# Optimization experiments

Hardware: AMD Instinct MI355X
Metric: run time of the kernel (lower is better)

Reference implementation:

```python
import jax, jax.numpy as jnp
import numpy as np

N_CIRC, N_MI, N_DIS = 40000, 15000, 8000
F_IN, HID, HEADS, OUT = 128, 64, 4, 64
E_CM, E_MD, E_CD = 400000, 300000, 300000
SIZES = (N_CIRC, N_MI, N_DIS)
# relation r: (src_type, dst_type) indices into [circ, mi, dis]
RELS = [(0, 1), (1, 2), (0, 2), (1, 0), (2, 1), (2, 0)]
EDGE_N = [E_CM, E_MD, E_CD, E_CM, E_MD, E_CD]


def _edges(k, n_src, n_dst, n_e):
    k1, k2 = jax.random.split(k)
    src = jax.random.randint(k1, (n_e,), 0, n_src, dtype=jnp.int32)
    dst = jax.random.randint(k2, (n_e,), 0, n_dst, dtype=jnp.int32)
    return jnp.stack([src, dst])


def setup_inputs() -> dict:
    key = jax.random.key(0)
    ks = jax.random.split(key, 20)
    x_circ = jax.random.normal(ks[0], (N_CIRC, F_IN), jnp.float32)
    x_mi = jax.random.normal(ks[1], (N_MI, F_IN), jnp.float32)
    x_dis = jax.random.normal(ks[2], (N_DIS, F_IN), jnp.float32)
    ed = [_edges(ks[3 + r], SIZES[RELS[r][0]], SIZES[RELS[r][1]], EDGE_N[r]) for r in range(6)]
    s1 = 1.0 / np.sqrt(F_IN)
    s2 = 1.0 / np.sqrt(HID * HEADS)
    W1 = jax.random.normal(ks[10], (6, F_IN, HEADS * HID), jnp.float32) * s1
    as1 = jax.random.normal(ks[11], (6, HEADS, HID), jnp.float32) * s2
    ad1 = jax.random.normal(ks[12], (6, HEADS, HID), jnp.float32) * s2
    b1 = jnp.zeros((6, HEADS * HID), jnp.float32)
    W2 = jax.random.normal(ks[13], (6, HEADS * HID, OUT), jnp.float32) * s2
    as2 = jax.random.normal(ks[14], (6, 1, OUT), jnp.float32) * s2
    ad2 = jax.random.normal(ks[15], (6, 1, OUT), jnp.float32) * s2
    b2 = jnp.zeros((6, OUT), jnp.float32)
    return {"x_circ": x_circ, "x_mi": x_mi, "x_dis": x_dis,
            "e_cm": ed[0], "e_md": ed[1], "e_cd": ed[2],
            "e_mc": ed[3], "e_dm": ed[4], "e_dc": ed[5],
            "W1": W1, "as1": as1, "ad1": ad1, "b1": b1,
            "W2": W2, "as2": as2, "ad2": ad2, "b2": b2}


def _gat(x_src, x_dst, src, dst, W, a_s, a_d, b, n_dst, concat):
    # PyG GATConv (shared lin for src/dst), add_self_loops=False, eval mode.
    H, C = a_s.shape
    h_src = (x_src @ W).reshape(-1, H, C)   # [Ns,H,C]
    h_dst = (x_dst @ W).reshape(-1, H, C)   # [Nd,H,C]
    al_s = jnp.einsum('nhc,hc->nh', h_src, a_s)
    al_d = jnp.einsum('nhc,hc->nh', h_dst, a_d)
    e = jax.nn.leaky_relu(al_s[src] + al_d[dst], 0.2)           # [E,H]
    m = jax.ops.segment_max(e, dst, num_segments=n_dst)         # [Nd,H]
    m = jnp.where(jnp.isfinite(m), m, 0.0)
    ex = jnp.exp(e - m[dst])
    den = jax.ops.segment_sum(ex, dst, num_segments=n_dst)
    alpha = ex / (den[dst] + 1e-16)                             # scatter-softmax
    msg = h_src[src] * alpha[:, :, None]                        # [E,H,C]
    out = jax.ops.segment_sum(msg.reshape(-1, H * C), dst, num_segments=n_dst)
    out = out.reshape(n_dst, H, C)
    return (out.reshape(n_dst, H * C) if concat else out.mean(axis=1)) + b


def _hetero(xs, edges, W, a_s, a_d, b, concat):
    acc = [[] for _ in xs]
    for r, (s, d) in enumerate(RELS):
        o = _gat(xs[s], xs[d], edges[r][0], edges[r][1], W[r], a_s[r], a_d[r], b[r], SIZES[d], concat)
        acc[d].append(o)
    return [jnp.mean(jnp.stack(lst), axis=0) for lst in acc]  # aggr='mean'


def reference(x_circ, x_mi, x_dis, e_cm, e_md, e_cd, e_mc, e_dm, e_dc,
              W1, as1, ad1, b1, W2, as2, ad2, b2):
    xs = [x_circ, x_mi, x_dis]
    edges = [e_cm, e_md, e_cd, e_mc, e_dm, e_dc]
    h = _hetero(xs, edges, W1, as1, ad1, b1, concat=True)
    h = [jax.nn.elu(v) for v in h]  # dropout is identity in eval
    h = _hetero(h, edges, W2, as2, ad2, b2, concat=False)
    out = [v / jnp.maximum(jnp.linalg.norm(v, axis=1, keepdims=True), 1e-12) for v in h]
    return tuple(out)
```

## Files before the change

kernel.cpp:

```cpp
#include <hip/hip_runtime.h>
#include <hip/hip_bf16.h>
#include <math.h>

#define NCIRC 40000
#define NMI   15000
#define NDIS  8000
#define NTOT  (NCIRC + NMI + NDIS)
#define OFFSTR 40064

typedef __hip_bfloat16 bf16;
typedef __attribute__((ext_vector_type(8))) short short8;
typedef __attribute__((ext_vector_type(4))) float f32x4;
typedef __attribute__((ext_vector_type(8))) unsigned short us8v;

static __device__ __forceinline__ float us2f(unsigned short u){ return __uint_as_float(((unsigned)u) << 16); }
static __device__ __forceinline__ unsigned short f2bu(float v){
    bf16 t = __float2bfloat16(v);
    return *reinterpret_cast<unsigned short*>(&t);
}
static __device__ __forceinline__ float ldx(const void* p, size_t i, int f32){
    return f32 ? ((const float*)p)[i] : __bfloat162float(((const bf16*)p)[i]);
}
static inline unsigned cdiv(long long a, long long b){ return (unsigned)((a + b - 1) / b); }

struct CsrArgs {
    const int* src[6]; const int* dst[6];
    int ecnt[6]; int eoff[6]; int nd[6];
};
struct Al1Args { const void* x[3]; const float* wa[3][4]; float* out[3][4]; int nt[3]; };
struct Al2Args { const unsigned short* x[3]; const float* wa[3][4]; float* out[3][4]; int nt[3]; };
struct GemmArgs { const void* A[6]; unsigned long long bOff[6]; unsigned long long cOff[6];
                  int M[6]; int nblk[6]; };
struct GatArgs {
    const unsigned short* srcs[3][2]; const int* off[3][2];
    const float* als[3][2]; const float* ald[3][2];
    const unsigned short* hs[3][2];
};
struct P1Args {
    CsrArgs ca;
    const void *W1, *as1, *ad1, *W2, *as2, *ad2, *b1, *b2;
    float *WA1S, *WA1D, *WA2S, *WA2D, *BIAS1, *BIAS2;
    bf16 *W1T, *W2T;
    int *CNT;
    int eTw1, eTw2, eWa1, eWa2, eBias;
    int nbCnt[6];
};
struct P2Args {
    CsrArgs ca;
    const int* OFF; int* POS; unsigned short* SRCS;
    GemmArgs g1;
    Al1Args a1;
    int eFill, eGemm;
    int nbCnt[6];
    int nbAl[3];
};
struct P3Args {
    Al2Args a2;
    GemmArgs g2;
    int eAl2;
    int nbAl[3];
};
struct P2ArgsFix { P2Args p; const bf16* W1T; bf16* HS1; };
struct P3ArgsFix { P3Args p; const bf16* W2T; bf16* HS2; };

__global__ void detect_dtype(const unsigned short* __restrict__ u, int* __restrict__ flag){
    int bad = 0;
    for (int i = threadIdx.x; i < 4096; i += 256){
        int e = (u[i] >> 7) & 0xFF;
        if (e >= 0x90) bad = 1;
    }
    if (bad) atomicOr(flag, 1);
}

static __device__ __forceinline__ void tw_body(const void* W, int f32, bf16* WT,
                                               int Kd, int Nd, int nrel, int blk){
    long long idx = (long long)blk * 256 + threadIdx.x;
    long long tot = (long long)nrel * Kd * Nd;
    if (idx >= tot) return;
    int per = Kd * Nd;
    int r = (int)(idx / per);
    int rem = (int)(idx % per);
    int n = rem / Kd, k = rem % Kd;
    float v = ldx(W, (size_t)r*per + (size_t)k*Nd + n, f32);
    WT[idx] = __float2bfloat16(v);
}

static __device__ __forceinline__ void wa1_body(const void* W1, const void* as1, const void* ad1,
                                                int f32, float* wa_s, float* wa_d, int blk){
    int r = blk >> 1;
    int t = (blk & 1)*256 + threadIdx.x;
    int f = t >> 2, h = t & 3;
    size_t wb = (size_t)r*128*256 + (size_t)f*256 + h*64;
    size_t ab = (size_t)r*256 + h*64;
    float ss = 0.f, sd = 0.f;
    for (int c = 0; c < 64; c++){
        float w = ldx(W1, wb + c, f32);
        ss += w * ldx(as1, ab + c, f32);
        sd += w * ldx(ad1, ab + c, f32);
    }
    wa_s[r*512 + t] = ss; wa_d[r*512 + t] = sd;
}

static __device__ __forceinline__ void wa2_body(const void* W2, const void* as2, const void* ad2,
                                                int f32, float* wa_s, float* wa_d, int r){
    int f = threadIdx.x;
    size_t wb = (size_t)r*256*64 + (size_t)f*64;
    float ss = 0.f, sd = 0.f;
    for (int c = 0; c < 64; c++){
        float w = ldx(W2, wb + c, f32);
        ss += w * ldx(as2, (size_t)r*64 + c, f32);
        sd += w * ldx(ad2, (size_t)r*64 + c, f32);
    }
    wa_s[r*256 + f] = ss; wa_d[r*256 + f] = sd;
}

static __device__ __forceinline__ void bias_body(const void* b1, const void* b2, int f32,
                                                 float* BIAS1, float* BIAS2, int t){
    const int relA[3] = {3, 0, 1};
    const int relB[3] = {5, 4, 2};
    int c = threadIdx.x;
    BIAS1[t*256 + c] = 0.5f*(ldx(b1, relA[t]*256 + c, f32) + ldx(b1, relB[t]*256 + c, f32));
    if (c < 64)
        BIAS2[t*64 + c] = 0.5f*(ldx(b2, relA[t]*64 + c, f32) + ldx(b2, relB[t]*64 + c, f32));
}

static __device__ void al1_body(const Al1Args& a, int f32, int t, int blk, float (*swa)[512]){
    int N = a.nt[t];
    for (int i = threadIdx.x; i < 2048; i += 256) swa[i >> 9][i & 511] = a.wa[t][i >> 9][i & 511];
    __syncthreads();
    int n = blk * 256 + threadIdx.x;
    if (n >= N) return;
    float s[4][4] = {};
    if (f32){
        const float* xr = (const float*)a.x[t] + (size_t)n*128;
        for (int f = 0; f < 128; f++){
            float v = xr[f];
            #pragma unroll
            for (int j = 0; j < 4; j++){
                s[j][0] += v*swa[j][f*4+0]; s[j][1] += v*swa[j][f*4+1];
                s[j][2] += v*swa[j][f*4+2]; s[j][3] += v*swa[j][f*4+3];
            }
        }
    } else {
        const unsigned short* xr = (const unsigned short*)a.x[t] + (size_t)n*128;
        for (int f0 = 0; f0 < 128; f0 += 8){
            us8v v8 = *(const us8v*)(xr + f0);
            #pragma unroll
            for (int jj = 0; jj < 8; jj++){
                float v = us2f(v8[jj]); int f = f0 + jj;
                #pragma unroll
                for (int j = 0; j < 4; j++){
                    s[j][0] += v*swa[j][f*4+0]; s[j][1] += v*swa[j][f*4+1];
                    s[j][2] += v*swa[j][f*4+2]; s[j][3] += v*swa[j][f*4+3];
                }
            }
        }
    }
    #pragma unroll
    for (int j = 0; j < 4; j++)
        *(float4*)(a.out[t][j] + (size_t)n*4) = make_float4(s[j][0], s[j][1], s[j][2], s[j][3]);
}

static __device__ void al2_body(const Al2Args& a, int t, int blk, float (*swa)[256]){
    int N = a.nt[t];
    for (int i = threadIdx.x; i < 1024; i += 256) swa[i >> 8][i & 255] = a.wa[t][i >> 8][i & 255];
    __syncthreads();
    int n = blk * 256 + threadIdx.x;
    if (n >= N) return;
    const unsigned short* xr = a.x[t] + (size_t)n*256;
    float s0 = 0.f, s1 = 0.f, s2 = 0.f, s3 = 0.f;
    for (int f0 = 0; f0 < 256; f0 += 8){
        us8v v8 = *(const us8v*)(xr + f0);
        #pragma unroll
        for (int jj = 0; jj < 8; jj++){
            float v = us2f(v8[jj]); int f = f0 + jj;
            s0 += v*swa[0][f]; s1 += v*swa[1][f]; s2 += v*swa[2][f]; s3 += v*swa[3][f];
        }
    }
    a.out[t][0][n] = s0; a.out[t][1][n] = s1; a.out[t][2][n] = s2; a.out[t][3][n] = s3;
}

static __device__ void gemm_body(const GemmArgs& ga, int af32, const bf16* WT,
                                 bf16* Cb, int N, int K, int nIdx, int yTot,
                                 unsigned short (*As)[40], unsigned short (*Bs)[40]){
    int y = yTot, r = 0;
    while (r < 5 && y >= ga.nblk[r]){ y -= ga.nblk[r]; r++; }
    int M = ga.M[r];
    int m0 = y * 64, n0 = nIdx * 64;
    const void* A = ga.A[r];
    const unsigned short* WTu = (const unsigned short*)WT + ga.bOff[r];
    bf16* C = Cb + ga.cOff[r];
    int tid = threadIdx.x;
    int w = tid >> 6, lane = tid & 63;
    int quad = lane >> 4, l16 = lane & 15;
    int srow = tid >> 2, skc = (tid & 3) * 8;
    f32x4 acc[4] = {};
    for (int k0 = 0; k0 < K; k0 += 32){
        {
            int gr = m0 + srow;
            us8v av;
            if (gr < M){
                if (af32){
                    const float* ap = (const float*)A + (size_t)gr*K + k0 + skc;
                    #pragma unroll
                    for (int j = 0; j < 8; j++) av[j] = f2bu(ap[j]);
                } else {
                    av = *(const us8v*)((const unsigned short*)A + (size_t)gr*K + k0 + skc);
                }
            } else {
                #pragma unroll
                for (int j = 0; j < 8; j++) av[j] = 0;
            }
            *(us8v*)&As[srow][skc] = av;
        }
        *(us8v*)&Bs[srow][skc] = *(const us8v*)(WTu + (size_t)(n0 + srow)*K + k0 + skc);
        __syncthreads();
        short8 af = *(const short8*)&As[w*16 + l16][quad*8];
        #pragma unroll
        for (int c = 0; c < 4; c++){
            short8 bfv = *(const short8*)&Bs[c*16 + l16][quad*8];
            acc[c] = __builtin_amdgcn_mfma_f32_16x16x32_bf16(af, bfv, acc[c], 0, 0, 0);
        }
        __syncthreads();
    }
    #pragma unroll
    for (int c = 0; c < 4; c++){
        #pragma unroll
        for (int i = 0; i < 4; i++){
            int m = m0 + w*16 + quad*4 + i;
            if (m < M) C[(size_t)m*N + n0 + c*16 + l16] = __float2bfloat16(acc[c][i]);
        }
    }
}

__global__ void p1_k(P1Args p, const int* __restrict__ flag){
    int bid = blockIdx.x;
    int f32 = *flag;
    if (bid < p.eTw1){
        tw_body(p.W1, f32, p.W1T, 128, 256, 6, bid);
    } else if (bid < p.eTw2){
        tw_body(p.W2, f32, p.W2T, 256, 64, 6, bid - p.eTw1);
    } else if (bid < p.eWa1){
        wa1_body(p.W1, p.as1, p.ad1, f32, p.WA1S, p.WA1D, bid - p.eTw2);
    } else if (bid < p.eWa2){
        wa2_body(p.W2, p.as2, p.ad2, f32, p.WA2S, p.WA2D, bid - p.eWa1);
    } else if (bid < p.eBias){
        bias_body(p.b1, p.b2, f32, p.BIAS1, p.BIAS2, bid - p.eWa2);
    } else {
        int b = bid - p.eBias, r = 0;
        while (r < 5 && b >= p.nbCnt[r]){ b -= p.nbCnt[r]; r++; }
        int e = b*256 + threadIdx.x;
        if (e < p.ca.ecnt[r]) atomicAdd(&p.CNT[r*OFFSTR + p.ca.dst[r][e]], 1);
    }
}

__global__ void csr_scan_all(CsrArgs a, const int* __restrict__ cnt, int* __restrict__ off){
    int r = blockIdx.x;
    int N = a.nd[r];
    const int* c = cnt + r*OFFSTR;
    int* o = off + r*OFFSTR;
    __shared__ int wsum[16];
    __shared__ int base;
    int tid = threadIdx.x, lane = tid & 63, wv = tid >> 6;
    if (tid == 0) base = 0;
    __syncthreads();
    for (int c0 = 0; c0 < N; c0 += 1024){
        int i = c0 + tid;
        int x = (i < N) ? c[i] : 0;
        #pragma unroll
        for (int d = 1; d < 64; d <<= 1){
            int y = __shfl_up(x, d, 64);
            if (lane >= d) x += y;
        }
        if (lane == 63) wsum[wv] = x;
        __syncthreads();
        if (tid == 0){
            int s = 0;
            #pragma unroll
            for (int k = 0; k < 16; k++){ s += wsum[k]; wsum[k] = s; }
        }
        __syncthreads();
        int woff = (wv == 0) ? 0 : wsum[wv - 1];
        if (i < N) o[i + 1] = base + woff + x;
        int total = wsum[15];
        __syncthreads();
        if (tid == 0) base += total;
        __syncthreads();
    }
    if (tid == 0) o[0] = 0;
}

__global__ void p2_kf(P2ArgsFix q, const int* __restrict__ flag){
    __shared__ __align__(16) char smem[10240];
    P2Args& p = q.p;
    int bid = blockIdx.x;
    if (bid < p.eFill){
        int b = bid, r = 0;
        while (r < 5 && b >= p.nbCnt[r]){ b -= p.nbCnt[r]; r++; }
        int e = b*256 + threadIdx.x;
        if (e < p.ca.ecnt[r]){
            int d = p.ca.dst[r][e];
            int pos = atomicAdd(&p.POS[r*OFFSTR + d], 1);
            p.SRCS[p.ca.eoff[r] + p.OFF[r*OFFSTR + d] + pos] = (unsigned short)p.ca.src[r][e];
        }
    } else if (bid < p.eGemm){
        int id = bid - p.eFill;
        int nIdx = id & 3, yTot = id >> 2;
        unsigned short (*As)[40] = (unsigned short(*)[40])smem;
        unsigned short (*Bs)[40] = (unsigned short(*)[40])(smem + 5120);
        gemm_body(p.g1, *flag, q.W1T, q.HS1, 256, 128, nIdx, yTot, As, Bs);
    } else {
        int b = bid - p.eGemm, t = 0;
        while (t < 2 && b >= p.nbAl[t]){ b -= p.nbAl[t]; t++; }
        al1_body(p.a1, *flag, t, b, (float(*)[512])smem);
    }
}

__global__ void p3_kf(P3ArgsFix q){
    __shared__ __align__(16) char smem[10240];
    P3Args& p = q.p;
    int bid = blockIdx.x;
    if (bid < p.eAl2){
        int b = bid, t = 0;
        while (t < 2 && b >= p.nbAl[t]){ b -= p.nbAl[t]; t++; }
        al2_body(p.a2, t, b, (float(*)[256])smem);
    } else {
        int yTot = bid - p.eAl2;
        unsigned short (*As)[40] = (unsigned short(*)[40])smem;
        unsigned short (*Bs)[40] = (unsigned short(*)[40])(smem + 5120);
        gemm_body(p.g2, 0, q.W2T, q.HS2, 64, 256, 0, yTot, As, Bs);
    }
}

__global__ void gat_l1(GatArgs g, const float* __restrict__ BIAS1,
                       unsigned short* __restrict__ X2B){
    int gw = blockIdx.x * 4 + (threadIdx.x >> 6);
    if (gw >= NTOT) return;
    int t, w;
    if (gw < NCIRC){ t = 0; w = gw; }
    else if (gw < NCIRC + NMI){ t = 1; w = gw - NCIRC; }
    else { t = 2; w = gw - NCIRC - NMI; }
    int lane = threadIdx.x & 63;
    int hw = lane >> 5, l32 = lane & 31;
    int h = l32 >> 3;
    float fT[8] = {0.f,0.f,0.f,0.f,0.f,0.f,0.f,0.f};
    #pragma unroll
    for (int a = 0; a < 2; a++){
        const float* als = g.als[t][a];
        const unsigned short* srcs = g.srcs[t][a];
        const unsigned short* Hu = g.hs[t][a];
        float aldv = g.ald[t][a][(size_t)w*4 + h];
        int beg = g.off[t][a][w], end = g.off[t][a][w+1];
        float fa[8] = {0.f,0.f,0.f,0.f,0.f,0.f,0.f,0.f};
        float den = 0.f;
        int i = beg + hw;
        for (; i + 6 < end; i += 8){
            int s0 = srcs[i], s1 = srcs[i+2], s2 = srcs[i+4], s3 = srcs[i+6];
            us8v v0 = *(const us8v*)(Hu + (size_t)s0*256 + l32*8);
            us8v v1 = *(const us8v*)(Hu + (size_t)s1*256 + l32*8);
            us8v v2 = *(const us8v*)(Hu + (size_t)s2*256 + l32*8);
            us8v v3 = *(const us8v*)(Hu + (size_t)s3*256 + l32*8);
            float x0 = als[(size_t)s0*4 + h] + aldv;
            float x1 = als[(size_t)s1*4 + h] + aldv;
            float x2 = als[(size_t)s2*4 + h] + aldv;
            float x3 = als[(size_t)s3*4 + h] + aldv;
            float e0 = __expf(x0 > 0.f ? x0 : 0.2f*x0);
            float e1 = __expf(x1 > 0.f ? x1 : 0.2f*x1);
            float e2 = __expf(x2 > 0.f ? x2 : 0.2f*x2);
            float e3 = __expf(x3 > 0.f ? x3 : 0.2f*x3);
            den += e0 + e1 + e2 + e3;
            #pragma unroll
            for (int k = 0; k < 8; k++)
                fa[k] += e0*us2f(v0[k]) + e1*us2f(v1[k]) + e2*us2f(v2[k]) + e3*us2f(v3[k]);
        }
        for (; i < end; i += 2){
            int s = srcs[i];
            us8v v = *(const us8v*)(Hu + (size_t)s*256 + l32*8);
            float xv = als[(size_t)s*4 + h] + aldv;
            float e = __expf(xv > 0.f ? xv : 0.2f*xv);
            den += e;
            #pragma unroll
            for (int k = 0; k < 8; k++) fa[k] += e*us2f(v[k]);
        }
        den += __shfl_xor(den, 32, 64);
        float inv = 1.0f / (den + 1e-16f);
        #pragma unroll
        for (int k = 0; k < 8; k++) fT[k] += fa[k]*inv;
    }
    #pragma unroll
    for (int k = 0; k < 8; k++) fT[k] += __shfl_xor(fT[k], 32, 64);
    if (hw == 0){
        const float* bp = BIAS1 + t*256 + l32*8;
        us8v st;
        #pragma unroll
        for (int k = 0; k < 8; k++){
            float v = fT[k]*0.5f + bp[k];
            v = v > 0.f ? v : (__expf(v) - 1.f);
            st[k] = f2bu(v);
        }
        *(us8v*)(X2B + (size_t)gw*256 + l32*8) = st;
    }
}

__global__ void gat_l2(GatArgs g, const float* __restrict__ BIAS2,
                       void* __restrict__ out, const int* __restrict__ flag){
    int gw = blockIdx.x * 4 + (threadIdx.x >> 6);
    if (gw >= NTOT) return;
    int t, w;
    if (gw < NCIRC){ t = 0; w = gw; }
    else if (gw < NCIRC + NMI){ t = 1; w = gw - NCIRC; }
    else { t = 2; w = gw - NCIRC - NMI; }
    int lane = threadIdx.x & 63;
    int qw = lane >> 4, l16 = lane & 15;
    float fT[4] = {0.f,0.f,0.f,0.f};
    #pragma unroll
    for (int a = 0; a < 2; a++){
        const float* als = g.als[t][a];
        const unsigned short* srcs = g.srcs[t][a];
        const unsigned short* Hu = g.hs[t][a];
        float aldv = g.ald[t][a][w];
        int beg = g.off[t][a][w], end = g.off[t][a][w+1];
        float fa[4] = {0.f,0.f,0.f,0.f};
        float den = 0.f;
        int i = beg + qw;
        for (; i + 12 < end; i += 16){
            int s0 = srcs[i], s1 = srcs[i+4], s2 = srcs[i+8], s3 = srcs[i+12];
            ushort4 v0 = *(const ushort4*)(Hu + (size_t)s0*64 + l16*4);
            ushort4 v1 = *(const ushort4*)(Hu + (size_t)s1*64 + l16*4);
            ushort4 v2 = *(const ushort4*)(Hu + (size_t)s2*64 + l16*4);
            ushort4 v3 = *(const ushort4*)(Hu + (size_t)s3*64 + l16*4);
            float x0 = als[s0] + aldv, x1 = als[s1] + aldv;
            float x2 = als[s2] + aldv, x3 = als[s3] + aldv;
            float e0 = __expf(x0 > 0.f ? x0 : 0.2f*x0);
            float e1 = __expf(x1 > 0.f ? x1 : 0.2f*x1);
            float e2 = __expf(x2 > 0.f ? x2 : 0.2f*x2);
            float e3 = __expf(x3 > 0.f ? x3 : 0.2f*x3);
            den += e0 + e1 + e2 + e3;
            fa[0] += e0*us2f(v0.x) + e1*us2f(v1.x) + e2*us2f(v2.x) + e3*us2f(v3.x);
            fa[1] += e0*us2f(v0.y) + e1*us2f(v1.y) + e2*us2f(v2.y) + e3*us2f(v3.y);
            fa[2] += e0*us2f(v0.z) + e1*us2f(v1.z) + e2*us2f(v2.z) + e3*us2f(v3.z);
            fa[3] += e0*us2f(v0.w) + e1*us2f(v1.w) + e2*us2f(v2.w) + e3*us2f(v3.w);
        }
        for (; i < end; i += 4){
            int s = srcs[i];
            ushort4 v = *(const ushort4*)(Hu + (size_t)s*64 + l16*4);
            float xv = als[s] + aldv;
            float e = __expf(xv > 0.f ? xv : 0.2f*xv);
            den += e;
            fa[0] += e*us2f(v.x); fa[1] += e*us2f(v.y);
            fa[2] += e*us2f(v.z); fa[3] += e*us2f(v.w);
        }
        den += __shfl_xor(den, 32, 64);
        den += __shfl_xor(den, 16, 64);
        float inv = 1.0f / (den + 1e-16f);
        #pragma unroll
        for (int k = 0; k < 4; k++) fT[k] += fa[k]*inv;
    }
    #pragma unroll
    for (int k = 0; k < 4; k++){
        fT[k] += __shfl_xor(fT[k], 32, 64);
        fT[k] += __shfl_xor(fT[k], 16, 64);
    }
    const float* bp = BIAS2 + t*64 + l16*4;
    float v0 = fT[0]*0.5f + bp[0];
    float v1 = fT[1]*0.5f + bp[1];
    float v2 = fT[2]*0.5f + bp[2];
    float v3 = fT[3]*0.5f + bp[3];
    float ss = v0*v0 + v1*v1 + v2*v2 + v3*v3;
    #pragma unroll
    for (int mk = 8; mk > 0; mk >>= 1) ss += __shfl_xor(ss, mk, 64);
    float nrm = sqrtf(ss);
    nrm = nrm > 1e-12f ? nrm : 1e-12f;
    float inv_n = 1.0f / nrm;
    if (qw == 0){
        size_t base = (size_t)gw*64 + l16*4;
        if (*flag){
            *(float4*)((float*)out + base) = make_float4(v0*inv_n, v1*inv_n, v2*inv_n, v3*inv_n);
        } else {
            ushort4 st;
            st.x = f2bu(v0*inv_n); st.y = f2bu(v1*inv_n);
            st.z = f2bu(v2*inv_n); st.w = f2bu(v3*inv_n);
            *(ushort4*)((unsigned short*)out + base) = st;
        }
    }
}

extern "C" void kernel_launch(void* const* d_in, const int* in_sizes, int n_in,
                              void* d_out, int out_size, void* d_ws, size_t ws_size,
                              hipStream_t stream){
    const void* x[3] = {d_in[0], d_in[1], d_in[2]};
    const int Nt[3] = {NCIRC, NMI, NDIS};
    const int* ep[6]; int Ecnt[6];
    for (int r = 0; r < 6; r++){ ep[r] = (const int*)d_in[3 + r]; Ecnt[r] = in_sizes[3 + r] / 2; }
    const void* W1  = d_in[9];
    const void* as1 = d_in[10];
    const void* ad1 = d_in[11];
    const void* b1  = d_in[12];
    const void* W2  = d_in[13];
    const void* as2 = d_in[14];
    const void* ad2 = d_in[15];
    const void* b2  = d_in[16];

    const int rs[6] = {0, 1, 0, 1, 2, 2};
    const int rd[6] = {1, 2, 2, 0, 1, 0};
    const int srel[3][2] = {{0, 2}, {1, 3}, {4, 5}};
    const int drel[3][2] = {{3, 5}, {0, 4}, {1, 2}};
    const int accRow[3] = {0, NCIRC, NCIRC + NMI};

    float* ws    = (float*)d_ws;
    int*   FLAG  = (int*)ws;
    float* WA1S  = ws + 16;
    float* WA1D  = WA1S + 6*512;
    float* WA2S  = WA1D + 6*512;
    float* WA2D  = WA2S + 6*256;
    float* BIAS1 = WA2D + 6*256;
    float* BIAS2 = BIAS1 + 768;
    float* ALB   = BIAS2 + 192;
    unsigned short* HS1u = (unsigned short*)(ALB + 1008000);
    unsigned short* HS2u = HS1u + 32256000;
    unsigned short* X2Bu = HS2u + 8064000;
    bf16*  W1T   = (bf16*)(X2Bu + 16128000);
    bf16*  W2T   = W1T + 6*256*128;
    int*   CNT   = (int*)(W2T + 6*64*256);
    int*   POS   = CNT + 6*OFFSTR;
    int*   OFF   = POS + 6*OFFSTR;
    unsigned short* SRCS = (unsigned short*)(OFF + 6*OFFSTR);

    int eOff[6]; int acc_e = 0;
    for (int r = 0; r < 6; r++){ eOff[r] = acc_e; acc_e += Ecnt[r]; }
    unsigned long long hs1off[6], hs2off[6];
    { unsigned long long o1 = 0, o2 = 0;
      for (int r = 0; r < 6; r++){ hs1off[r] = o1; o1 += (unsigned long long)Nt[rs[r]]*256;
                                   hs2off[r] = o2; o2 += (unsigned long long)Nt[rs[r]]*64; } }
    float *AL1S[6], *AL1D[6], *AL2S[6], *AL2D[6];
    { size_t o = 0;
      for (int r = 0; r < 6; r++){ AL1S[r] = ALB + o; o += (size_t)Nt[rs[r]]*4; }
      for (int r = 0; r < 6; r++){ AL1D[r] = ALB + o; o += (size_t)Nt[rd[r]]*4; }
      size_t o2 = 0;
      for (int r = 0; r < 6; r++){ AL2S[r] = ALB + o2; o2 += (size_t)Nt[rs[r]]; }
      for (int r = 0; r < 6; r++){ AL2D[r] = ALB + o2; o2 += (size_t)Nt[rd[r]]; } }

    CsrArgs ca;
    for (int r = 0; r < 6; r++){
        ca.src[r] = ep[r]; ca.dst[r] = ep[r] + Ecnt[r];
        ca.ecnt[r] = Ecnt[r]; ca.eoff[r] = eOff[r]; ca.nd[r] = Nt[rd[r]];
    }

    hipMemsetAsync(FLAG, 0, sizeof(int), stream);
    hipMemsetAsync(CNT, 0, (size_t)12*OFFSTR*sizeof(int), stream);
    detect_dtype<<<1, 256, 0, stream>>>((const unsigned short*)d_in[0], FLAG);

    P1Args p1;
    p1.ca = ca;
    p1.W1 = W1; p1.as1 = as1; p1.ad1 = ad1; p1.W2 = W2; p1.as2 = as2; p1.ad2 = ad2;
    p1.b1 = b1; p1.b2 = b2;
    p1.WA1S = WA1S; p1.WA1D = WA1D; p1.WA2S = WA2S; p1.WA2D = WA2D;
    p1.BIAS1 = BIAS1; p1.BIAS2 = BIAS2;
    p1.W1T = W1T; p1.W2T = W2T; p1.CNT = CNT;
    int nTw1 = cdiv(6LL*128*256, 256), nTw2 = cdiv(6LL*256*64, 256);
    p1.eTw1 = nTw1; p1.eTw2 = nTw1 + nTw2;
    p1.eWa1 = p1.eTw2 + 12; p1.eWa2 = p1.eWa1 + 6; p1.eBias = p1.eWa2 + 3;
    int cntBlk = 0;
    for (int r = 0; r < 6; r++){ p1.nbCnt[r] = cdiv(Ecnt[r], 256); cntBlk += p1.nbCnt[r]; }
    p1_k<<<p1.eBias + cntBlk, 256, 0, stream>>>(p1, FLAG);

    csr_scan_all<<<6, 1024, 0, stream>>>(ca, CNT, OFF);

    P2ArgsFix q2;
    q2.p.ca = ca; q2.p.OFF = OFF; q2.p.POS = POS; q2.p.SRCS = SRCS;
    int totBlk1 = 0;
    for (int r = 0; r < 6; r++){
        q2.p.g1.A[r] = x[rs[r]]; q2.p.g1.bOff[r] = (unsigned long long)r*256*128;
        q2.p.g1.cOff[r] = hs1off[r]; q2.p.g1.M[r] = Nt[rs[r]];
        q2.p.g1.nblk[r] = cdiv(Nt[rs[r]], 64); totBlk1 += q2.p.g1.nblk[r];
        q2.p.nbCnt[r] = p1.nbCnt[r];
    }
    for (int t = 0; t < 3; t++){
        q2.p.a1.x[t] = x[t]; q2.p.a1.nt[t] = Nt[t];
        q2.p.nbAl[t] = cdiv(Nt[t], 256);
        for (int j = 0; j < 2; j++){
            q2.p.a1.wa[t][j]   = WA1S + srel[t][j]*512;  q2.p.a1.out[t][j]   = AL1S[srel[t][j]];
            q2.p.a1.wa[t][j+2] = WA1D + drel[t][j]*512;  q2.p.a1.out[t][j+2] = AL1D[drel[t][j]];
        }
    }
    q2.p.eFill = cntBlk; q2.p.eGemm = cntBlk + 4*totBlk1;
    q2.W1T = W1T; q2.HS1 = (bf16*)HS1u;
    int nAl1 = q2.p.nbAl[0] + q2.p.nbAl[1] + q2.p.nbAl[2];
    p2_kf<<<q2.p.eGemm + nAl1, 256, 0, stream>>>(q2, FLAG);

    GatArgs gl1;
    for (int t = 0; t < 3; t++)
        for (int a = 0; a < 2; a++){
            int r = drel[t][a];
            gl1.srcs[t][a] = SRCS + eOff[r]; gl1.off[t][a] = OFF + r*OFFSTR;
            gl1.als[t][a] = AL1S[r]; gl1.ald[t][a] = AL1D[r];
            gl1.hs[t][a] = HS1u + hs1off[r];
        }
    gat_l1<<<cdiv(NTOT, 4), 256, 0, stream>>>(gl1, BIAS1, X2Bu);

    P3ArgsFix q3;
    int totBlk2 = 0;
    for (int r = 0; r < 6; r++){
        q3.p.g2.A[r] = X2Bu + (size_t)accRow[rs[r]]*256;
        q3.p.g2.bOff[r] = (unsigned long long)r*64*256;
        q3.p.g2.cOff[r] = hs2off[r]; q3.p.g2.M[r] = Nt[rs[r]];
        q3.p.g2.nblk[r] = cdiv(Nt[rs[r]], 64); totBlk2 += q3.p.g2.nblk[r];
    }
    for (int t = 0; t < 3; t++){
        q3.p.a2.x[t] = X2Bu + (size_t)accRow[t]*256; q3.p.a2.nt[t] = Nt[t];
        q3.p.nbAl[t] = cdiv(Nt[t], 256);
        for (int j = 0; j < 2; j++){
            q3.p.a2.wa[t][j]   = WA2S + srel[t][j]*256;  q3.p.a2.out[t][j]   = AL2S[srel[t][j]];
            q3.p.a2.wa[t][j+2] = WA2D + drel[t][j]*256;  q3.p.a2.out[t][j+2] = AL2D[drel[t][j]];
        }
    }
    q3.p.eAl2 = q3.p.nbAl[0] + q3.p.nbAl[1] + q3.p.nbAl[2];
    q3.W2T = W2T; q3.HS2 = (bf16*)HS2u;
    p3_kf<<<q3.p.eAl2 + totBlk2, 256, 0, stream>>>(q3);

    GatArgs gl2;
    for (int t = 0; t < 3; t++)
        for (int a = 0; a < 2; a++){
            int r = drel[t][a];
            gl2.srcs[t][a] = SRCS + eOff[r]; gl2.off[t][a] = OFF + r*OFFSTR;
            gl2.als[t][a] = AL2S[r]; gl2.ald[t][a] = AL2D[r];
            gl2.hs[t][a] = HS2u + hs2off[r];
        }
    gat_l2<<<cdiv(NTOT, 4), 256, 0, stream>>>(gl2, BIAS2, d_out, FLAG);
}
```

Before: 634.2 us.

## Parallelize CSR offset scan across chunks and fuse init memsets into one kernel

Replaces the single-block-per-relation sequential CSR prefix scan with a three-phase chunked scan (per-chunk scan, chunk-total scan, add-back) spread over many blocks. It also merges the flag and count memsets with the dtype detection into one init kernel. The goal is to remove a serial scan over up to 40 chunks per relation and some launch overhead. The cost is two extra kernel launches for the scan phases and an extra pass over the offsets.

```diff
diff --git a/kernel.cpp b/kernel.cpp
--- a/kernel.cpp
+++ b/kernel.cpp
@@ -27,6 +27,7 @@
     const int* src[6]; const int* dst[6];
     int ecnt[6]; int eoff[6]; int nd[6];
 };
+struct ScanArgs { int start[6]; int nch[6]; int nd[6]; };
 struct Al1Args { const void* x[3]; const float* wa[3][4]; float* out[3][4]; int nt[3]; };
 struct Al2Args { const unsigned short* x[3]; const float* wa[3][4]; float* out[3][4]; int nt[3]; };
 struct GemmArgs { const void* A[6]; unsigned long long bOff[6]; unsigned long long cOff[6];
@@ -63,13 +64,24 @@
 struct P2ArgsFix { P2Args p; const bf16* W1T; bf16* HS1; };
 struct P3ArgsFix { P3Args p; const bf16* W2T; bf16* HS2; };
 
-__global__ void detect_dtype(const unsigned short* __restrict__ u, int* __restrict__ flag){
-    int bad = 0;
-    for (int i = threadIdx.x; i < 4096; i += 256){
-        int e = (u[i] >> 7) & 0xFF;
-        if (e >= 0x90) bad = 1;
-    }
-    if (bad) atomicOr(flag, 1);
+__global__ void init_k(const unsigned short* __restrict__ u, int* __restrict__ flag,
+                       int* __restrict__ zbase, int zcount){
+    if (blockIdx.x == 0){
+        __shared__ int sbad;
+        if (threadIdx.x == 0) sbad = 0;
+        __syncthreads();
+        int bad = 0;
+        for (int i = threadIdx.x; i < 4096; i += 256){
+            int e = (u[i] >> 7) & 0xFF;
+            if (e >= 0x90) bad = 1;
+        }
+        if (bad) atomicOr(&sbad, 1);
+        __syncthreads();
+        if (threadIdx.x == 0) *flag = sbad;
+    } else {
+        for (int i = (blockIdx.x - 1)*256 + threadIdx.x; i < zcount; i += 63*256)
+            zbase[i] = 0;
+    }
 }
 
 static __device__ __forceinline__ void tw_body(const void* W, int f32, bf16* WT,
@@ -254,40 +266,55 @@
     }
 }
 
-__global__ void csr_scan_all(CsrArgs a, const int* __restrict__ cnt, int* __restrict__ off){
-    int r = blockIdx.x;
-    int N = a.nd[r];
-    const int* c = cnt + r*OFFSTR;
-    int* o = off + r*OFFSTR;
+__global__ void scan_a(ScanArgs s, const int* __restrict__ cnt, int* __restrict__ off,
+                       int* __restrict__ CHT){
+    int b = blockIdx.x, r = 0;
+    while (r < 5 && b >= s.start[r+1]) r++;
+    int chunk = b - s.start[r];
+    int N = s.nd[r];
+    int tid = threadIdx.x, lane = tid & 63, wv = tid >> 6;
     __shared__ int wsum[16];
-    __shared__ int base;
-    int tid = threadIdx.x, lane = tid & 63, wv = tid >> 6;
-    if (tid == 0) base = 0;
+    int i = chunk*1024 + tid;
+    int x = (i < N) ? cnt[r*OFFSTR + i] : 0;
+    #pragma unroll
+    for (int d = 1; d < 64; d <<= 1){
+        int y = __shfl_up(x, d, 64);
+        if (lane >= d) x += y;
+    }
+    if (lane == 63) wsum[wv] = x;
     __syncthreads();
-    for (int c0 = 0; c0 < N; c0 += 1024){
-        int i = c0 + tid;
-        int x = (i < N) ? c[i] : 0;
+    if (tid == 0){
+        int acc = 0;
         #pragma unroll
-        for (int d = 1; d < 64; d <<= 1){
-            int y = __shfl_up(x, d, 64);
-            if (lane >= d) x += y;
-        }
-        if (lane == 63) wsum[wv] = x;
-        __syncthreads();
-        if (tid == 0){
-            int s = 0;
-            #pragma unroll
-            for (int k = 0; k < 16; k++){ s += wsum[k]; wsum[k] = s; }
-        }
-        __syncthreads();
-        int woff = (wv == 0) ? 0 : wsum[wv - 1];
-        if (i < N) o[i + 1] = base + woff + x;
-        int total = wsum[15];
-        __syncthreads();
-        if (tid == 0) base += total;
-        __syncthreads();
-    }
-    if (tid == 0) o[0] = 0;
+        for (int k = 0; k < 16; k++){ acc += wsum[k]; wsum[k] = acc; }
+    }
+    __syncthreads();
+    int incl = x + ((wv == 0) ? 0 : wsum[wv - 1]);
+    if (i < N) off[r*OFFSTR + i + 1] = incl;
+    if (tid == 1023) CHT[r*64 + chunk] = incl;
+}
+
+__global__ void scan_b(ScanArgs s, int* __restrict__ CHT){
+    int r = threadIdx.x;
+    if (r < 6){
+        int acc = 0;
+        for (int c = 0; c < s.nch[r]; c++){
+            int v = CHT[r*64 + c];
+            CHT[r*64 + c] = acc;
+            acc += v;
+        }
+    }
+}
+
+__global__ void scan_c(ScanArgs s, int* __restrict__ off, const int* __restrict__ CHT){
+    int b = blockIdx.x, r = 0;
+    while (r < 5 && b >= s.start[r+1]) r++;
+    int chunk = b - s.start[r];
+    int N = s.nd[r];
+    int i = chunk*1024 + threadIdx.x;
+    int addv = CHT[r*64 + chunk];
+    if (i < N) off[r*OFFSTR + i + 1] += addv;
+    if (chunk == 0 && threadIdx.x == 0) off[r*OFFSTR] = 0;
 }
 
 __global__ void p2_kf(P2ArgsFix q, const int* __restrict__ flag){
@@ -524,7 +551,8 @@
     int*   CNT   = (int*)(W2T + 6*64*256);
     int*   POS   = CNT + 6*OFFSTR;
     int*   OFF   = POS + 6*OFFSTR;
-    unsigned short* SRCS = (unsigned short*)(OFF + 6*OFFSTR);
+    int*   CHT   = OFF + 6*OFFSTR;
+    unsigned short* SRCS = (unsigned short*)(CHT + 6*64);
 
     int eOff[6]; int acc_e = 0;
     for (int r = 0; r < 6; r++){ eOff[r] = acc_e; acc_e += Ecnt[r]; }
@@ -546,9 +574,7 @@
         ca.ecnt[r] = Ecnt[r]; ca.eoff[r] = eOff[r]; ca.nd[r] = Nt[rd[r]];
     }
 
-    hipMemsetAsync(FLAG, 0, sizeof(int), stream);
-    hipMemsetAsync(CNT, 0, (size_t)12*OFFSTR*sizeof(int), stream);
-    detect_dtype<<<1, 256, 0, stream>>>((const unsigned short*)d_in[0], FLAG);
+    init_k<<<64, 256, 0, stream>>>((const unsigned short*)d_in[0], FLAG, CNT, 12*OFFSTR);
 
     P1Args p1;
     p1.ca = ca;
@@ -564,7 +590,17 @@
     for (int r = 0; r < 6; r++){ p1.nbCnt[r] = cdiv(Ecnt[r], 256); cntBlk += p1.nbCnt[r]; }
     p1_k<<<p1.eBias + cntBlk, 256, 0, stream>>>(p1, FLAG);
 
-    csr_scan_all<<<6, 1024, 0, stream>>>(ca, CNT, OFF);
+    ScanArgs sa;
+    int scBlk = 0;
+    for (int r = 0; r < 6; r++){
+        sa.start[r] = scBlk;
+        sa.nd[r] = Nt[rd[r]];
+        sa.nch[r] = cdiv(Nt[rd[r]], 1024);
+        scBlk += sa.nch[r];
+    }
+    scan_a<<<scBlk, 1024, 0, stream>>>(sa, CNT, OFF, CHT);
+    scan_b<<<1, 64, 0, stream>>>(sa, CHT);
+    scan_c<<<scBlk, 1024, 0, stream>>>(sa, OFF, CHT);
 
     P2ArgsFix q2;
     q2.p.ca = ca; q2.p.OFF = OFF; q2.p.POS = POS; q2.p.SRCS = SRCS;
```

Measured after the change: 607.4 us. -4.2%, faster.
